# Performance work log

Hardware: AMD Instinct MI355X
Metric: run time of the kernel (lower is better)

## Reference

```python
import jax, jax.numpy as jnp
import numpy as np

H = 16        # query heads
HK = 8        # key/value heads
HD = 128      # head dim
EPS = 1e-6
THETA = 1000000.0


def _rmsnorm(x, w):
    # per-head RMSNorm over last dim (head_dim)
    var = jnp.mean(jnp.square(x.astype(jnp.float32)), axis=-1, keepdims=True)
    return (x * jax.lax.rsqrt(var + EPS)).astype(x.dtype) * w


def _rope(x, cos, sin):
    # x: [B, S, h, HD]; cos/sin: [S, HD//2]
    x1, x2 = jnp.split(x, 2, axis=-1)
    c = cos[None, :, None, :]
    s = sin[None, :, None, :]
    return jnp.concatenate([x1 * c - x2 * s, x2 * c + x1 * s], axis=-1)


def setup_inputs() -> dict:
    key = jax.random.key(0)
    ks = jax.random.split(key, 5)
    B, S, D = 2, 2048, 2048
    scale = 0.02
    return {
        "x": jax.random.normal(ks[0], (B, S, D), jnp.float32),
        "wq": jax.random.normal(ks[1], (H * HD, D), jnp.float32) * scale,
        "wk": jax.random.normal(ks[2], (HK * HD, D), jnp.float32) * scale,
        "wv": jax.random.normal(ks[3], (HK * HD, D), jnp.float32) * scale,
        "wo": jax.random.normal(ks[4], (D, H * HD), jnp.float32) * scale,
        "q_norm_w": jnp.ones((HD,), jnp.float32),
        "k_norm_w": jnp.ones((HD,), jnp.float32),
    }


def reference(x, wq, wk, wv, wo, q_norm_w, k_norm_w):
    B, S, D = x.shape
    # QKV projections (no bias)
    q = (x @ wq.T).reshape(B, S, H, HD)
    k = (x @ wk.T).reshape(B, S, HK, HD)
    v = (x @ wv.T).reshape(B, S, HK, HD)

    # per-head RMSNorm on Q and K (Qwen3 qk-norm)
    q = _rmsnorm(q, q_norm_w)
    k = _rmsnorm(k, k_norm_w)

    # RoPE
    inv_freq = 1.0 / (THETA ** (jnp.arange(0, HD, 2, dtype=jnp.float32) / HD))
    ang = jnp.arange(S, dtype=jnp.float32)[:, None] * inv_freq[None, :]  # [S, HD/2]
    cos, sin = jnp.cos(ang), jnp.sin(ang)
    q = _rope(q, cos, sin)
    k = _rope(k, cos, sin)

    # GQA: repeat KV heads to match query heads
    rep = H // HK
    k = jnp.repeat(k, rep, axis=2)  # [B, S, H, HD]
    v = jnp.repeat(v, rep, axis=2)

    # causal SDPA
    scores = jnp.einsum("bqhd,bkhd->bhqk", q, k) / jnp.sqrt(jnp.float32(HD))
    mask = jnp.tril(jnp.ones((S, S), dtype=bool))
    scores = jnp.where(mask[None, None], scores, jnp.finfo(scores.dtype).min)
    probs = jax.nn.softmax(scores, axis=-1)
    out = jnp.einsum("bhqk,bkhd->bqhd", probs, v).reshape(B, S, H * HD)

    return out @ wo.T
```

## Files before the change

kernel.cpp:

```cpp
#include <hip/hip_runtime.h>
#include <hip/hip_bf16.h>
#include <math.h>

#define B_   2
#define S_   2048
#define D_   2048
#define H_   16
#define HK_  8
#define HD_  128
#define BS_  (B_ * S_)
#define NQKV 4096
#define SCALE 0.08838834764831845f

typedef __bf16 bf16x8 __attribute__((ext_vector_type(8)));
typedef __bf16 bf16x4 __attribute__((ext_vector_type(4)));
typedef float  f32x4  __attribute__((ext_vector_type(4)));

#define AS1(p) ((const __attribute__((address_space(1))) void*)(p))
#define AS3(p) ((__attribute__((address_space(3))) void*)(p))

template <int S>
__device__ __forceinline__ float ror16(float x) {
    return __builtin_bit_cast(float, __builtin_amdgcn_update_dpp(
        0, __builtin_bit_cast(int, x), 0x120 | S, 0xF, 0xF, true));
}
__device__ __forceinline__ float row_sum16(float x) {
    x += ror16<8>(x);
    x += ror16<4>(x);
    x += ror16<2>(x);
    x += ror16<1>(x);
    return x;
}

__global__ __launch_bounds__(256) void cvt_all(const float* __restrict__ x,
                                               const float* __restrict__ wq,
                                               const float* __restrict__ wk,
                                               const float* __restrict__ wv,
                                               const float* __restrict__ wo,
                                               __bf16* __restrict__ xb,
                                               __bf16* __restrict__ wb,
                                               __bf16* __restrict__ wob) {
    int bid = blockIdx.x;
    const float* src;
    __bf16* dst;
    int i4;
    if (bid < 8192)       { src = x;  dst = xb;                    i4 = bid * 256; }
    else if (bid < 12288) { src = wq; dst = wb;                    i4 = (bid - 8192) * 256; }
    else if (bid < 14336) { src = wk; dst = wb + (size_t)4194304;  i4 = (bid - 12288) * 256; }
    else if (bid < 16384) { src = wv; dst = wb + (size_t)6291456;  i4 = (bid - 14336) * 256; }
    else                  { src = wo; dst = wob;                   i4 = (bid - 16384) * 256; }
    i4 += threadIdx.x;
    float4 v = reinterpret_cast<const float4*>(src)[i4];
    bf16x4 o = {(__bf16)v.x, (__bf16)v.y, (__bf16)v.z, (__bf16)v.w};
    reinterpret_cast<bf16x4*>(dst)[i4] = o;
}

__global__ __launch_bounds__(128) void build_rope(float* __restrict__ tab) {
    int s = blockIdx.x;
    int d = threadIdx.x;
    int i = d & 63;
    float inv_freq = exp2f(-19.931568569324174f * (float)(2 * i) * (1.0f / 128.0f));
    float ang = (float)s * inv_freq;
    float sn, cs;
    sincosf(ang, &sn, &cs);
    tab[s * 128 + d] = (d < 64) ? cs : sn;
}

template <typename CT>
__global__ __launch_bounds__(256) void gemm_bf16_nt(const __bf16* __restrict__ A,
                                                    const __bf16* __restrict__ W,
                                                    CT* __restrict__ C,
                                                    int M, int N, int K) {
    __shared__ __bf16 As[128 * 64];
    __shared__ __bf16 Bs[128 * 64];

    const int t    = threadIdx.x;
    const int w    = t >> 6;
    const int lane = t & 63;
    const int col  = lane & 15;
    const int quad = lane >> 4;
    const int wm   = w >> 1;
    const int wn   = w & 1;

    const int m0 = blockIdx.y * 128;
    const int n0 = blockIdx.x * 128;

    const int lrow8 = lane >> 3;
    const int lch   = ((lane & 7) ^ lrow8) * 8;

    const __bf16* agp = A + (size_t)(m0 + w * 32 + lrow8) * K + lch;
    const __bf16* wgp = W + (size_t)(n0 + w * 32 + lrow8) * K + lch;
    __bf16* alp = As + (w * 32) * 64;
    __bf16* blp = Bs + (w * 32) * 64;

    const int c7 = col & 7;

    f32x4 acc[4][4];
    #pragma unroll
    for (int m = 0; m < 4; m++)
        #pragma unroll
        for (int n = 0; n < 4; n++) acc[m][n] = (f32x4){0.f, 0.f, 0.f, 0.f};

    #pragma unroll 1
    for (int k0 = 0; k0 < K; k0 += 64) {
        #pragma unroll
        for (int j = 0; j < 4; j++) {
            __builtin_amdgcn_global_load_lds(AS1(agp + k0 + (size_t)(j * 8) * K),
                                             AS3(alp + j * 512), 16, 0, 0);
            __builtin_amdgcn_global_load_lds(AS1(wgp + k0 + (size_t)(j * 8) * K),
                                             AS3(blp + j * 512), 16, 0, 0);
        }
        __syncthreads();

        #pragma unroll
        for (int kk = 0; kk < 2; kk++) {
            bf16x8 af[4], bfr[4];
            #pragma unroll
            for (int m = 0; m < 4; m++)
                af[m] = *reinterpret_cast<const bf16x8*>(
                    &As[(wm * 64 + m * 16 + col) * 64 + ((kk * 4 + quad) ^ c7) * 8]);
            #pragma unroll
            for (int n = 0; n < 4; n++)
                bfr[n] = *reinterpret_cast<const bf16x8*>(
                    &Bs[(wn * 64 + n * 16 + col) * 64 + ((kk * 4 + quad) ^ c7) * 8]);

            #pragma unroll
            for (int m = 0; m < 4; m++)
                #pragma unroll
                for (int n = 0; n < 4; n++)
                    acc[m][n] = __builtin_amdgcn_mfma_f32_16x16x32_bf16(af[m], bfr[n], acc[m][n], 0, 0, 0);
        }
        __syncthreads();
    }

    #pragma unroll
    for (int m = 0; m < 4; m++) {
        #pragma unroll
        for (int r = 0; r < 4; r++) {
            size_t row = m0 + wm * 64 + m * 16 + quad * 4 + r;
            CT* cp = C + row * N + n0 + wn * 64 + col;
            #pragma unroll
            for (int n = 0; n < 4; n++) cp[n * 16] = (CT)acc[m][n][r];
        }
    }
}

template <typename CT>
__global__ __launch_bounds__(256) void gemm_bf16_nt_n64(const __bf16* __restrict__ A,
                                                        const __bf16* __restrict__ W,
                                                        CT* __restrict__ C,
                                                        int M, int N, int K) {
    __shared__ __bf16 As[128 * 64];
    __shared__ __bf16 Bs[64 * 64];

    const int t    = threadIdx.x;
    const int w    = t >> 6;
    const int lane = t & 63;
    const int col  = lane & 15;
    const int quad = lane >> 4;
    const int wm   = w >> 1;
    const int wn   = w & 1;

    const int m0 = blockIdx.x * 128;
    const int n0 = blockIdx.y * 64;

    const int lrow8 = lane >> 3;
    const int lch   = ((lane & 7) ^ lrow8) * 8;

    const __bf16* agp = A + (size_t)(m0 + w * 32 + lrow8) * K + lch;
    const __bf16* wgp = W + (size_t)(n0 + w * 16 + lrow8) * K + lch;
    __bf16* alp = As + (w * 32) * 64;
    __bf16* blp = Bs + (w * 16) * 64;

    const int c7 = col & 7;

    f32x4 acc[4][2];
    #pragma unroll
    for (int m = 0; m < 4; m++)
        #pragma unroll
        for (int n = 0; n < 2; n++) acc[m][n] = (f32x4){0.f, 0.f, 0.f, 0.f};

    #pragma unroll 1
    for (int k0 = 0; k0 < K; k0 += 64) {
        #pragma unroll
        for (int j = 0; j < 4; j++)
            __builtin_amdgcn_global_load_lds(AS1(agp + k0 + (size_t)(j * 8) * K),
                                             AS3(alp + j * 512), 16, 0, 0);
        #pragma unroll
        for (int j = 0; j < 2; j++)
            __builtin_amdgcn_global_load_lds(AS1(wgp + k0 + (size_t)(j * 8) * K),
                                             AS3(blp + j * 512), 16, 0, 0);
        __syncthreads();

        #pragma unroll
        for (int kk = 0; kk < 2; kk++) {
            bf16x8 af[4], bfr[2];
            #pragma unroll
            for (int m = 0; m < 4; m++)
                af[m] = *reinterpret_cast<const bf16x8*>(
                    &As[(wm * 64 + m * 16 + col) * 64 + ((kk * 4 + quad) ^ c7) * 8]);
            #pragma unroll
            for (int n = 0; n < 2; n++)
                bfr[n] = *reinterpret_cast<const bf16x8*>(
                    &Bs[(wn * 32 + n * 16 + col) * 64 + ((kk * 4 + quad) ^ c7) * 8]);

            #pragma unroll
            for (int m = 0; m < 4; m++)
                #pragma unroll
                for (int n = 0; n < 2; n++)
                    acc[m][n] = __builtin_amdgcn_mfma_f32_16x16x32_bf16(af[m], bfr[n], acc[m][n], 0, 0, 0);
        }
        __syncthreads();
    }

    #pragma unroll
    for (int m = 0; m < 4; m++) {
        #pragma unroll
        for (int r = 0; r < 4; r++) {
            size_t row = m0 + wm * 64 + m * 16 + quad * 4 + r;
            CT* cp = C + row * N + n0 + wn * 32 + col;
            #pragma unroll
            for (int n = 0; n < 2; n++) cp[n * 16] = (CT)acc[m][n][r];
        }
    }
}

__global__ __launch_bounds__(256) void norm_rope(__bf16* __restrict__ qkv,
                                                 const float* __restrict__ qw,
                                                 const float* __restrict__ kw,
                                                 const float* __restrict__ tab) {
    const int g    = blockIdx.x * 16 + (threadIdx.x >> 4);
    const int l    = threadIdx.x & 15;
    const int row  = g / 24;
    const int head = g - row * 24;
    const int s    = row & (S_ - 1);

    const float* w = (head < H_) ? qw : kw;
    __bf16* p = qkv + (size_t)row * NQKV + head * HD_ + l * 8;

    bf16x8 xv = *reinterpret_cast<const bf16x8*>(p);
    float xf[8];
    float ss = 0.f;
    #pragma unroll
    for (int j = 0; j < 8; j++) { xf[j] = (float)xv[j]; ss = fmaf(xf[j], xf[j], ss); }
    ss = row_sum16(ss);
    float rs = rsqrtf(ss * (1.0f / 128.0f) + 1e-6f);

    float nf[8];
    const float4 w0 = *reinterpret_cast<const float4*>(&w[l * 8]);
    const float4 w1 = *reinterpret_cast<const float4*>(&w[l * 8 + 4]);
    nf[0] = xf[0] * rs * w0.x; nf[1] = xf[1] * rs * w0.y;
    nf[2] = xf[2] * rs * w0.z; nf[3] = xf[3] * rs * w0.w;
    nf[4] = xf[4] * rs * w1.x; nf[5] = xf[5] * rs * w1.y;
    nf[6] = xf[6] * rs * w1.z; nf[7] = xf[7] * rs * w1.w;

    float of[8];
    #pragma unroll
    for (int j = 0; j < 8; j++) of[j] = __shfl_xor(nf[j], 8);

    const int ib = (l & 7) * 8;
    const float4 c0 = *reinterpret_cast<const float4*>(&tab[s * 128 + ib]);
    const float4 c1 = *reinterpret_cast<const float4*>(&tab[s * 128 + ib + 4]);
    const float4 s0 = *reinterpret_cast<const float4*>(&tab[s * 128 + 64 + ib]);
    const float4 s1 = *reinterpret_cast<const float4*>(&tab[s * 128 + 64 + ib + 4]);
    float cs[8] = {c0.x, c0.y, c0.z, c0.w, c1.x, c1.y, c1.z, c1.w};
    float sn[8] = {s0.x, s0.y, s0.z, s0.w, s1.x, s1.y, s1.z, s1.w};

    bf16x8 out;
    if (l < 8) {
        #pragma unroll
        for (int j = 0; j < 8; j++) out[j] = (__bf16)(nf[j] * cs[j] - of[j] * sn[j]);
    } else {
        #pragma unroll
        for (int j = 0; j < 8; j++) out[j] = (__bf16)(of[j] * sn[j] + nf[j] * cs[j]);
    }
    *reinterpret_cast<bf16x8*>(p) = out;
}

__global__ __launch_bounds__(256) void transpose_v(const __bf16* __restrict__ qkv,
                                                   __bf16* __restrict__ vt) {
    __shared__ __bf16 Ls[64][136];
    const int t  = threadIdx.x;
    const int bk = blockIdx.y;
    const int b  = bk >> 3;
    const int kvh = bk & 7;
    const int s0 = blockIdx.x * 64;

    #pragma unroll
    for (int i = 0; i < 4; i++) {
        int f = t + i * 256;
        int row = f >> 4;
        int d8 = (f & 15) * 8;
        bf16x8 v = *reinterpret_cast<const bf16x8*>(
            &qkv[(size_t)(b * S_ + s0 + row) * NQKV + 3072 + kvh * HD_ + d8]);
        *reinterpret_cast<bf16x8*>(&Ls[row][d8]) = v;
    }
    __syncthreads();

    #pragma unroll
    for (int i = 0; i < 4; i++) {
        int f = t + i * 256;
        int dim = f >> 3;
        int kc = f & 7;
        bf16x8 o;
        #pragma unroll
        for (int e = 0; e < 8; e++) o[e] = Ls[kc * 8 + e][dim];
        *reinterpret_cast<bf16x8*>(
            &vt[((size_t)bk * HD_ + dim) * S_ + s0 + kc * 8]) = o;
    }
}

__global__ __launch_bounds__(256) void attn_mfma(const __bf16* __restrict__ qkv,
                                                 const __bf16* __restrict__ vt,
                                                 __bf16* __restrict__ ao) {
    __shared__ __align__(16) char smem[17408];
    __bf16 (*Qs)[136] = reinterpret_cast<__bf16(*)[136]>(smem);
    __bf16 (*Ks)[136] = reinterpret_cast<__bf16(*)[136]>(smem);
    __shared__ __bf16 Vt[128][72];
    __shared__ __bf16 Ps[4][16][72];

    const int t    = threadIdx.x;
    const int w    = t >> 6;
    const int lane = t & 63;
    const int col  = lane & 15;
    const int quad = lane >> 4;

    const int bh  = blockIdx.x;
    const int b   = bh >> 4;
    const int h   = bh & 15;
    const int kvh = h >> 1;
    const int qb  = gridDim.y - 1 - blockIdx.y;
    const int r0  = qb * 64;

    const float C0 = SCALE * 1.44269504f;
    const float CM = -12.0f * 1.44269504f;

    const __bf16* vbase = vt + ((size_t)(b * HK_ + kvh) * HD_) * S_;

    const __bf16* kp[4];
    __bf16*       kw_[4];
    const __bf16* vp[4];
    __bf16*       vw_[4];
    #pragma unroll
    for (int i = 0; i < 4; i++) {
        int f = t + i * 256;
        int row = f >> 4, d8 = (f & 15) * 8;
        kp[i]  = qkv + (size_t)(b * S_ + row) * NQKV + 2048 + kvh * HD_ + d8;
        kw_[i] = &Ks[row][d8];
        int dim = f >> 3, kc = f & 7;
        vp[i]  = vbase + (size_t)dim * S_ + kc * 8;
        vw_[i] = &Vt[dim][kc * 8];
    }

    bf16x8 kreg[4], vreg[4];
    #pragma unroll
    for (int i = 0; i < 4; i++) {
        kreg[i] = *reinterpret_cast<const bf16x8*>(kp[i]);  kp[i] += (size_t)64 * NQKV;
        vreg[i] = *reinterpret_cast<const bf16x8*>(vp[i]);  vp[i] += 64;
    }

    #pragma unroll
    for (int i = 0; i < 4; i++) {
        int f   = t + i * 256;
        int row = f >> 4;
        int d8  = (f & 15) * 8;
        bf16x8 v = *reinterpret_cast<const bf16x8*>(
            &qkv[(size_t)(b * S_ + r0 + row) * NQKV + h * HD_ + d8]);
        *reinterpret_cast<bf16x8*>(&Qs[row][d8]) = v;
    }
    __syncthreads();

    bf16x8 qf[4];
    {
        const int m = w * 16 + col;
        #pragma unroll
        for (int k = 0; k < 4; k++)
            qf[k] = *reinterpret_cast<const bf16x8*>(&Qs[m][k * 32 + quad * 8]);
    }

    f32x4 o_acc[8];
    #pragma unroll
    for (int i = 0; i < 8; i++) o_acc[i] = (f32x4){0.f, 0.f, 0.f, 0.f};
    float l_lane[4] = {0.f, 0.f, 0.f, 0.f};

    const int ntiles = qb + 1;
    for (int ti = 0; ti < ntiles; ti++) {
        __syncthreads();

        #pragma unroll
        for (int i = 0; i < 4; i++) {
            *reinterpret_cast<bf16x8*>(kw_[i]) = kreg[i];
            *reinterpret_cast<bf16x8*>(vw_[i]) = vreg[i];
        }
        if (ti + 1 < ntiles) {
            #pragma unroll
            for (int i = 0; i < 4; i++) {
                kreg[i] = *reinterpret_cast<const bf16x8*>(kp[i]);  kp[i] += (size_t)64 * NQKV;
                vreg[i] = *reinterpret_cast<const bf16x8*>(vp[i]);  vp[i] += 64;
            }
        }
        __syncthreads();

        f32x4 s[4];
        #pragma unroll
        for (int n = 0; n < 4; n++) {
            f32x4 acc = (f32x4){0.f, 0.f, 0.f, 0.f};
            #pragma unroll
            for (int k = 0; k < 4; k++) {
                bf16x8 bf = *reinterpret_cast<const bf16x8*>(
                    &Ks[n * 16 + col][k * 32 + quad * 8]);
                acc = __builtin_amdgcn_mfma_f32_16x16x32_bf16(qf[k], bf, acc, 0, 0, 0);
            }
            s[n] = acc;
        }

        const bool diag = (ti == qb);
        #pragma unroll
        for (int r = 0; r < 4; r++) {
            float p0 = exp2f(fmaf(s[0][r], C0, CM));
            float p1 = exp2f(fmaf(s[1][r], C0, CM));
            float p2 = exp2f(fmaf(s[2][r], C0, CM));
            float p3 = exp2f(fmaf(s[3][r], C0, CM));
            if (diag) {
                int qloc = w * 16 + quad * 4 + r;
                if (0 * 16 + col > qloc) p0 = 0.f;
                if (1 * 16 + col > qloc) p1 = 0.f;
                if (2 * 16 + col > qloc) p2 = 0.f;
                if (3 * 16 + col > qloc) p3 = 0.f;
            }
            l_lane[r] += p0 + p1 + p2 + p3;
            Ps[w][quad * 4 + r][0 * 16 + col] = (__bf16)p0;
            Ps[w][quad * 4 + r][1 * 16 + col] = (__bf16)p1;
            Ps[w][quad * 4 + r][2 * 16 + col] = (__bf16)p2;
            Ps[w][quad * 4 + r][3 * 16 + col] = (__bf16)p3;
        }

        bf16x8 pf[2];
        #pragma unroll
        for (int ks = 0; ks < 2; ks++)
            pf[ks] = *reinterpret_cast<const bf16x8*>(&Ps[w][col][ks * 32 + quad * 8]);
        #pragma unroll
        for (int n = 0; n < 8; n++) {
            #pragma unroll
            for (int ks = 0; ks < 2; ks++) {
                bf16x8 vf = *reinterpret_cast<const bf16x8*>(
                    &Vt[n * 16 + col][ks * 32 + quad * 8]);
                o_acc[n] = __builtin_amdgcn_mfma_f32_16x16x32_bf16(pf[ks], vf, o_acc[n], 0, 0, 0);
            }
        }
    }

    #pragma unroll
    for (int r = 0; r < 4; r++) {
        float l = row_sum16(l_lane[r]);
        float inv = 1.0f / l;
        int qrow = r0 + w * 16 + quad * 4 + r;
        __bf16* op = ao + (size_t)(b * S_ + qrow) * (H_ * HD_) + h * HD_ + col;
        #pragma unroll
        for (int n = 0; n < 8; n++)
            op[n * 16] = (__bf16)(o_acc[n][r] * inv);
    }
}

extern "C" void kernel_launch(void* const* d_in, const int* in_sizes, int n_in,
                              void* d_out, int out_size, void* d_ws, size_t ws_size,
                              hipStream_t stream) {
    const float* x  = (const float*)d_in[0];
    const float* wq = (const float*)d_in[1];
    const float* wk = (const float*)d_in[2];
    const float* wv = (const float*)d_in[3];
    const float* wo = (const float*)d_in[4];
    const float* qw = (const float*)d_in[5];
    const float* kw = (const float*)d_in[6];
    float* out = (float*)d_out;

    __bf16* ws  = (__bf16*)d_ws;
    __bf16* xb  = ws;
    __bf16* wb  = xb  + (size_t)8388608;
    __bf16* wob = wb  + (size_t)8388608;
    __bf16* qkv = wob + (size_t)4194304;
    __bf16* ao  = qkv + (size_t)16777216;
    __bf16* vtg = ao  + (size_t)8388608;
    float* rtab = (float*)ao;

    cvt_all<<<20480, 256, 0, stream>>>(x, wq, wk, wv, wo, xb, wb, wob);
    build_rope<<<S_, 128, 0, stream>>>(rtab);

    gemm_bf16_nt<__bf16><<<dim3(NQKV / 128, BS_ / 128), 256, 0, stream>>>(
        xb, wb, qkv, BS_, NQKV, D_);

    norm_rope<<<(BS_ * 24) / 16, 256, 0, stream>>>(qkv, qw, kw, rtab);

    transpose_v<<<dim3(S_ / 64, B_ * HK_), 256, 0, stream>>>(qkv, vtg);

    attn_mfma<<<dim3(B_ * H_, S_ / 64), 256, 0, stream>>>(qkv, vtg, ao);

    gemm_bf16_nt_n64<float><<<dim3(BS_ / 128, D_ / 64), 256, 0, stream>>>(
        ao, wob, out, BS_, D_, H_ * HD_);
}
```

Before: 348.9 us.

## Replace QKV GEMM with 256x256-tile, 8-wave double-buffered phased pipeline

The QKV projection GEMM moves from a 128x128 tile with 4 waves and a load-sync-compute loop to a 256x256 tile with 8 waves. LDS is double-buffered, and each k-step is split into phases that interleave global-to-LDS staging of the next tile with MFMA work, using explicit barriers, waitcnt and setprio. The aim is to hide memory latency and raise data reuse per block. In exchange it uses much more LDS and registers, and for this shape the grid shrinks to 16x16 blocks, which may leave CUs underfilled.

```diff
diff --git a/kernel.cpp b/kernel.cpp
--- a/kernel.cpp
+++ b/kernel.cpp
@@ -66,81 +66,153 @@
     tab[s * 128 + d] = (d < 64) ? cs : sn;
 }
 
-template <typename CT>
-__global__ __launch_bounds__(256) void gemm_bf16_nt(const __bf16* __restrict__ A,
-                                                    const __bf16* __restrict__ W,
-                                                    CT* __restrict__ C,
-                                                    int M, int N, int K) {
-    __shared__ __bf16 As[128 * 64];
-    __shared__ __bf16 Bs[128 * 64];
+__global__ __launch_bounds__(512, 2) void gemm_bf16_8ph(const __bf16* __restrict__ A,
+                                                        const __bf16* __restrict__ W,
+                                                        __bf16* __restrict__ C,
+                                                        int M, int N, int K) {
+    __shared__ __bf16 lds[2][2][256 * 64];
 
     const int t    = threadIdx.x;
     const int w    = t >> 6;
     const int lane = t & 63;
     const int col  = lane & 15;
     const int quad = lane >> 4;
-    const int wm   = w >> 1;
-    const int wn   = w & 1;
-
-    const int m0 = blockIdx.y * 128;
-    const int n0 = blockIdx.x * 128;
-
-    const int lrow8 = lane >> 3;
-    const int lch   = ((lane & 7) ^ lrow8) * 8;
-
-    const __bf16* agp = A + (size_t)(m0 + w * 32 + lrow8) * K + lch;
-    const __bf16* wgp = W + (size_t)(n0 + w * 32 + lrow8) * K + lch;
-    __bf16* alp = As + (w * 32) * 64;
-    __bf16* blp = Bs + (w * 32) * 64;
-
-    const int c7 = col & 7;
-
-    f32x4 acc[4][4];
-    #pragma unroll
-    for (int m = 0; m < 4; m++)
-        #pragma unroll
-        for (int n = 0; n < 4; n++) acc[m][n] = (f32x4){0.f, 0.f, 0.f, 0.f};
+    const int c7   = col & 7;
+    const int wm   = w >> 2;
+    const int wn   = w & 3;
+
+    const int m0 = blockIdx.y * 256;
+    const int n0 = blockIdx.x * 256;
+
+    const int lr8 = lane >> 3;
+    const int sw8 = ((lane & 7) ^ lr8) * 8;
+    const __bf16* Ag = A + (size_t)(m0 + w * 16 + lr8) * K + sw8;
+    const __bf16* Wg = W + (size_t)(n0 + w * 16 + lr8) * K + sw8;
+
+    const int nkt = K >> 6;
+    const int nit = nkt >> 1;
+
+    const int aBase = (wm * 128 + col) * 64;
+    const int bBase = (wn * 64 + col) * 64;
+    const int kx0 = (quad ^ c7) * 8;
+    const int kx1 = ((4 + quad) ^ c7) * 8;
+
+    f32x4 acc[8][4];
+    #pragma unroll
+    for (int i = 0; i < 8; i++)
+        #pragma unroll
+        for (int j = 0; j < 4; j++) acc[i][j] = (f32x4){0.f, 0.f, 0.f, 0.f};
+
+    bf16x8 a[4][2], a2[4][2], b[2][2];
+
+    auto stg = [&](int ktv, int bufc, int ab, int half) {
+        if (ktv >= nkt) return;
+        const __bf16* gb = (ab ? Wg : Ag) + (size_t)half * 128 * K + (size_t)ktv * 64;
+        __bf16* db = &lds[bufc][ab][(half * 128 + w * 16) * 64];
+        __builtin_amdgcn_global_load_lds(AS1(gb), AS3(db), 16, 0, 0);
+        __builtin_amdgcn_global_load_lds(AS1(gb + (size_t)8 * K), AS3(db + 512), 16, 0, 0);
+    };
+    auto lda = [&](bf16x8 (&dst)[4][2], const __bf16* panel, int g) {
+        #pragma unroll
+        for (int mi = 0; mi < 4; mi++) {
+            dst[mi][0] = *reinterpret_cast<const bf16x8*>(&panel[aBase + (g * 64 + mi * 16) * 64 + kx0]);
+            dst[mi][1] = *reinterpret_cast<const bf16x8*>(&panel[aBase + (g * 64 + mi * 16) * 64 + kx1]);
+        }
+    };
+    auto ldb = [&](const __bf16* panel, int ng) {
+        #pragma unroll
+        for (int ni = 0; ni < 2; ni++) {
+            b[ni][0] = *reinterpret_cast<const bf16x8*>(&panel[bBase + (ng * 32 + ni * 16) * 64 + kx0]);
+            b[ni][1] = *reinterpret_cast<const bf16x8*>(&panel[bBase + (ng * 32 + ni * 16) * 64 + kx1]);
+        }
+    };
+    auto mm = [&](bf16x8 (&af)[4][2], int g, int ng) {
+        __builtin_amdgcn_s_setprio(1);
+        #pragma unroll
+        for (int mi = 0; mi < 4; mi++)
+            #pragma unroll
+            for (int ni = 0; ni < 2; ni++) {
+                f32x4 c = acc[g * 4 + mi][ng * 2 + ni];
+                c = __builtin_amdgcn_mfma_f32_16x16x32_bf16(af[mi][0], b[ni][0], c, 0, 0, 0);
+                c = __builtin_amdgcn_mfma_f32_16x16x32_bf16(af[mi][1], b[ni][1], c, 0, 0, 0);
+                acc[g * 4 + mi][ng * 2 + ni] = c;
+            }
+        __builtin_amdgcn_s_setprio(0);
+    };
+
+#define BARS do { __builtin_amdgcn_s_barrier(); __builtin_amdgcn_sched_barrier(0); } while (0)
+#define LGKM0 asm volatile("s_waitcnt lgkmcnt(0)" ::: "memory")
+
+    stg(0, 0, 0, 0); stg(0, 0, 0, 1); stg(0, 0, 1, 0); stg(0, 0, 1, 1);
+    stg(1, 1, 0, 0); stg(1, 1, 0, 1);
+    asm volatile("s_waitcnt vmcnt(4)" ::: "memory");
+    BARS;
 
     #pragma unroll 1
-    for (int k0 = 0; k0 < K; k0 += 64) {
-        #pragma unroll
-        for (int j = 0; j < 4; j++) {
-            __builtin_amdgcn_global_load_lds(AS1(agp + k0 + (size_t)(j * 8) * K),
-                                             AS3(alp + j * 512), 16, 0, 0);
-            __builtin_amdgcn_global_load_lds(AS1(wgp + k0 + (size_t)(j * 8) * K),
-                                             AS3(blp + j * 512), 16, 0, 0);
-        }
-        __syncthreads();
-
-        #pragma unroll
-        for (int kk = 0; kk < 2; kk++) {
-            bf16x8 af[4], bfr[4];
-            #pragma unroll
-            for (int m = 0; m < 4; m++)
-                af[m] = *reinterpret_cast<const bf16x8*>(
-                    &As[(wm * 64 + m * 16 + col) * 64 + ((kk * 4 + quad) ^ c7) * 8]);
-            #pragma unroll
-            for (int n = 0; n < 4; n++)
-                bfr[n] = *reinterpret_cast<const bf16x8*>(
-                    &Bs[(wn * 64 + n * 16 + col) * 64 + ((kk * 4 + quad) ^ c7) * 8]);
-
-            #pragma unroll
-            for (int m = 0; m < 4; m++)
-                #pragma unroll
-                for (int n = 0; n < 4; n++)
-                    acc[m][n] = __builtin_amdgcn_mfma_f32_16x16x32_bf16(af[m], bfr[n], acc[m][n], 0, 0, 0);
-        }
-        __syncthreads();
-    }
-
-    #pragma unroll
-    for (int m = 0; m < 4; m++) {
+    for (int it = 0; it < nit; ++it) {
+        const int k2 = it * 2;
+        const bool last = (it == nit - 1);
+
+        const __bf16* A0p = &lds[0][0][0];
+        const __bf16* B0p = &lds[0][1][0];
+        const __bf16* A1p = &lds[1][0][0];
+        const __bf16* B1p = &lds[1][1][0];
+
+        lda(a, A0p, 0); ldb(B0p, 0);
+        stg(k2 + 1, 1, 1, 0);
+        BARS; LGKM0;
+        mm(a, 0, 0);
+        BARS;
+        lda(a2, A0p, 1);
+        stg(k2 + 1, 1, 1, 1);
+        BARS; LGKM0;
+        mm(a2, 1, 0);
+        BARS;
+        ldb(B0p, 1);
+        stg(k2 + 2, 0, 0, 0);
+        BARS; LGKM0;
+        mm(a, 0, 1);
+        BARS;
+        stg(k2 + 2, 0, 0, 1);
+        BARS;
+        mm(a2, 1, 1);
+        if (last) { asm volatile("s_waitcnt vmcnt(0)" ::: "memory"); }
+        else      { asm volatile("s_waitcnt vmcnt(4)" ::: "memory"); }
+        BARS;
+
+        lda(a, A1p, 0); ldb(B1p, 0);
+        stg(k2 + 2, 0, 1, 0);
+        BARS; LGKM0;
+        mm(a, 0, 0);
+        BARS;
+        lda(a2, A1p, 1);
+        stg(k2 + 2, 0, 1, 1);
+        BARS; LGKM0;
+        mm(a2, 1, 0);
+        BARS;
+        ldb(B1p, 1);
+        stg(k2 + 3, 1, 0, 0);
+        BARS; LGKM0;
+        mm(a, 0, 1);
+        BARS;
+        stg(k2 + 3, 1, 0, 1);
+        BARS;
+        mm(a2, 1, 1);
+        if (!last) { asm volatile("s_waitcnt vmcnt(4)" ::: "memory"); }
+        BARS;
+    }
+
+#undef BARS
+#undef LGKM0
+
+    #pragma unroll
+    for (int m8 = 0; m8 < 8; m8++) {
         #pragma unroll
         for (int r = 0; r < 4; r++) {
-            size_t row = m0 + wm * 64 + m * 16 + quad * 4 + r;
-            CT* cp = C + row * N + n0 + wn * 64 + col;
-            #pragma unroll
-            for (int n = 0; n < 4; n++) cp[n * 16] = (CT)acc[m][n][r];
+            size_t row = m0 + wm * 128 + m8 * 16 + quad * 4 + r;
+            __bf16* cp = C + row * N + n0 + wn * 64 + col;
+            #pragma unroll
+            for (int n4 = 0; n4 < 4; n4++) cp[n4 * 16] = (__bf16)acc[m8][n4][r];
         }
     }
 }
@@ -486,7 +558,7 @@
     cvt_all<<<20480, 256, 0, stream>>>(x, wq, wk, wv, wo, xb, wb, wob);
     build_rope<<<S_, 128, 0, stream>>>(rtab);
 
-    gemm_bf16_nt<__bf16><<<dim3(NQKV / 128, BS_ / 128), 256, 0, stream>>>(
+    gemm_bf16_8ph<<<dim3(NQKV / 256, BS_ / 256), 512, 0, stream>>>(
         xb, wb, qkv, BS_, NQKV, D_);
 
     norm_rope<<<(BS_ * 24) / 16, 256, 0, stream>>>(qkv, qw, kw, rtab);
```

Result: faster. 335.1 us (-3.9%).
